# Kernel tuning notes

Measured on AMD Instinct MI355X. Metric: run time of the kernel, lower is better.

The kernel has to match this reference:

```python
import jax, jax.numpy as jnp
import numpy as np

WS = 8            # window_size
SHIFT = WS // 2   # shift_size


def _relative_position_index(ws):
    coords = np.stack(np.meshgrid(np.arange(ws), np.arange(ws), indexing='ij'))  # (2, ws, ws)
    coords = coords.reshape(2, -1)                        # (2, ws^2)
    rel = coords[:, :, None] - coords[:, None, :]          # (2, ws^2, ws^2)
    rel = rel.transpose(1, 2, 0)
    rel[:, :, 0] += ws - 1
    rel[:, :, 1] += ws - 1
    rel[:, :, 0] *= 2 * ws - 1
    return rel.sum(-1).astype(np.int32)                   # (ws^2, ws^2)


def _shift_mask(H, W, ws, shift):
    # Swin-style region-id mask for shifted windows -> bool (nh, nw, ws^2, ws^2)
    img = np.zeros((H, W), dtype=np.int32)
    cnt = 0
    sl = (slice(0, -ws), slice(-ws, -shift), slice(-shift, None))
    for hs in sl:
        for wsl in sl:
            img[hs, wsl] = cnt
            cnt += 1
    nh, nw = H // ws, W // ws
    win = img.reshape(nh, ws, nw, ws).transpose(0, 2, 1, 3).reshape(nh, nw, ws * ws)
    return win[:, :, :, None] != win[:, :, None, :]


def setup_inputs() -> dict:
    key = jax.random.key(0)
    ks = jax.random.split(key, 6)
    B, H, W, D, NHEAD = 8, 256, 256, 96, 6
    x = jax.random.normal(ks[0], (B, H, W, D), dtype=jnp.float32)
    w_qkv = jax.random.normal(ks[1], (D, 3 * D), dtype=jnp.float32) * 0.05
    b_qkv = jnp.zeros((3 * D,), dtype=jnp.float32)
    w_out = jax.random.normal(ks[2], (D, D), dtype=jnp.float32) * 0.05
    b_out = jnp.zeros((D,), dtype=jnp.float32)
    rpe_table = jax.random.normal(ks[3], ((2 * WS - 1) ** 2, NHEAD), dtype=jnp.float32) * 0.02
    rp_index = jnp.asarray(_relative_position_index(WS))
    mask = jnp.asarray(_shift_mask(H, W, WS, SHIFT))
    return {"x": x, "w_qkv": w_qkv, "b_qkv": b_qkv, "w_out": w_out,
            "b_out": b_out, "rpe_table": rpe_table, "rp_index": rp_index, "mask": mask}


def _partition(t, ws):
    # (B, h, H, W, dk) -> (B, h, nh, nw, ws*ws, dk)
    B, h, H, W, dk = t.shape
    nh, nw = H // ws, W // ws
    t = t.reshape(B, h, nh, ws, nw, ws, dk).transpose(0, 1, 2, 4, 3, 5, 6)
    return t.reshape(B, h, nh, nw, ws * ws, dk)


def _merge(t, ws):
    # inverse of _partition -> (B, h, H, W, dk)
    B, h, nh, nw, _, dk = t.shape
    t = t.reshape(B, h, nh, nw, ws, ws, dk).transpose(0, 1, 2, 4, 3, 5, 6)
    return t.reshape(B, h, nh * ws, nw * ws, dk)


def reference(x, w_qkv, b_qkv, w_out, b_out, rpe_table, rp_index, mask):
    B, H, W, D = x.shape
    n_head = rpe_table.shape[1]
    d_k = D // n_head
    scale = 1.0 / np.sqrt(d_k)
    ws2 = mask.shape[-1]
    ws = int(round(ws2 ** 0.5))
    shift = ws // 2

    qkv = (x @ w_qkv + b_qkv).reshape(B, H, W, 3, n_head, d_k)
    qkv = qkv.transpose(3, 0, 4, 1, 2, 5)          # (3, B, h, H, W, dk)
    q, k, v = qkv[0], qkv[1], qkv[2]

    # cyclic shift
    q = jnp.roll(q, (-shift, -shift), axis=(2, 3))
    k = jnp.roll(k, (-shift, -shift), axis=(2, 3))
    v = jnp.roll(v, (-shift, -shift), axis=(2, 3))

    q = _partition(q, ws)                          # (B, h, nh, nw, ws^2, dk)
    k = _partition(k, ws)
    v = _partition(v, ws)

    scores = jnp.einsum('bhijqd,bhijkd->bhijqk', q, k) * scale
    bias = rpe_table[rp_index]                     # (ws^2, ws^2, h)
    scores = scores + bias.transpose(2, 0, 1)[None, :, None, None]
    scores = jnp.where(mask[None, None], -1e9, scores)
    attn = jax.nn.softmax(scores, axis=-1)

    out = jnp.einsum('bhijqk,bhijkd->bhijqd', attn, v)
    out = _merge(out, ws)                          # (B, h, H, W, dk)
    out = jnp.roll(out, (shift, shift), axis=(2, 3))
    out = out.transpose(0, 2, 3, 1, 4).reshape(B, H, W, D)
    return out @ w_out + b_out
```

## Files before the change

kernel.cpp:

```cpp
#include <hip/hip_runtime.h>
#include <stdint.h>

#define HH    256
#define DD    96
#define NH    6
#define WSZ   8

typedef __bf16 bf16_t;
typedef bf16_t bf16x8 __attribute__((ext_vector_type(8)));
typedef short  s16x4  __attribute__((ext_vector_type(4)));
typedef float  f32x4  __attribute__((ext_vector_type(4)));

union U2  { bf16_t h[2]; uint32_t u; };
union Upk { uint32_t u[2]; s16x4 s; };

#define LOG2E 1.44269504088896f

static __device__ __forceinline__ uint32_t pack2(float a, float b) {
    U2 x; x.h[0] = (bf16_t)a; x.h[1] = (bf16_t)b; return x.u;
}

static __device__ __forceinline__ f32x4 mfma16(s16x4 a, s16x4 b, f32x4 c) {
#if __has_builtin(__builtin_amdgcn_mfma_f32_16x16x16bf16_1k)
    return __builtin_amdgcn_mfma_f32_16x16x16bf16_1k(a, b, c, 0, 0, 0);
#else
    f32x4 d;
    asm volatile("v_mfma_f32_16x16x16_bf16 %0, %1, %2, %3"
                 : "=v"(d) : "v"(a), "v"(b), "v"(c));
    return d;
#endif
}

static __device__ __forceinline__ float fast_exp2(float x) {
#if __has_builtin(__builtin_amdgcn_exp2f)
    return __builtin_amdgcn_exp2f(x);
#else
    return exp2f(x);
#endif
}

static __device__ __forceinline__ float fast_rcp(float x) {
#if __has_builtin(__builtin_amdgcn_rcpf)
    return __builtin_amdgcn_rcpf(x);
#else
    return 1.0f / x;
#endif
}

#define OFF_WQT_HI 0
#define OFF_WQT_LO 36864
#define OFF_WV_HI  73728
#define OFF_WV_LO  92160
#define OFF_WO_HI  110592
#define OFF_WO_LO  129024
#define OFF_RPE    147456

static __device__ __forceinline__ int swz(int row, int col) {
    return row * 128 + ((((col >> 3) ^ (row & 15)) & 15) << 3) + (col & 7);
}

__global__ __launch_bounds__(256)
void prep_kernel(const float* __restrict__ wqkv, const float* __restrict__ wout,
                 const float* __restrict__ rpe, char* __restrict__ ws)
{
    bf16_t* wqt_hi = (bf16_t*)(ws + OFF_WQT_HI);
    bf16_t* wqt_lo = (bf16_t*)(ws + OFF_WQT_LO);
    bf16_t* wv_hi  = (bf16_t*)(ws + OFF_WV_HI);
    bf16_t* wv_lo  = (bf16_t*)(ws + OFF_WV_LO);
    bf16_t* wo_hi  = (bf16_t*)(ws + OFF_WO_HI);
    bf16_t* wo_lo  = (bf16_t*)(ws + OFF_WO_LO);
    float*  rpe_b  = (float*)(ws + OFF_RPE);

    int idx = blockIdx.x * 256 + threadIdx.x;
    {
        int j = idx & 7, lane = (idx >> 3) & 63, frag = idx >> 9;
        int c = lane & 15, g = lane >> 4;
        if (idx < 18432) {
            int ks = frag % 3, r2 = frag / 3, wh = r2 % 6, t = r2 / 6;
            int k = ks * 32 + g * 8 + j;
            float v = wqkv[k * 288 + t * 96 + wh * 16 + c];
            bf16_t h = (bf16_t)v;
            wqt_hi[idx] = h;
            wqt_lo[idx] = (bf16_t)(v - (float)h);
        }
        if (idx < 9216) {
            int ks = frag % 3, wh = frag / 3;
            int k = ks * 32 + g * 8 + j;
            float v = wqkv[k * 288 + 192 + wh * 16 + c];
            bf16_t h = (bf16_t)v;
            wv_hi[idx] = h;
            wv_lo[idx] = (bf16_t)(v - (float)h);
            float v2 = wout[k * 96 + wh * 16 + c];
            bf16_t h2 = (bf16_t)v2;
            wo_hi[idx] = h2;
            wo_lo[idx] = (bf16_t)(v2 - (float)h2);
        }
    }
    if (idx < 24576) {
        int i = idx & 3, lane = (idx >> 2) & 63, kt = (idx >> 8) & 3,
            nt = (idx >> 10) & 3, h = idx >> 12;
        int c = lane & 15, g = lane >> 4;
        int k = kt * 16 + g * 4 + i, q = nt * 16 + c;
        int qr = q >> 3, qc = q & 7, kr = k >> 3, kc = k & 7;
        rpe_b[idx] = rpe[((qr - kr + 7) * 15 + (qc - kc + 7)) * NH + h] * LOG2E;
    }
}

__global__ __launch_bounds__(768, 4)
void swin_mfma(const float* __restrict__ x,
               const float* __restrict__ b_qkv,
               const float* __restrict__ b_out,
               const char*  __restrict__ ws,
               float* __restrict__ out)
{
    __shared__ char smem[65536];

    const int tid  = threadIdx.x;
    const int w2   = tid >> 6;
    const int wv   = (w2 >= 6) ? 1 : 0;
    const int w    = w2 - 6 * wv;
    const int lane = tid & 63;
    const int g    = lane >> 4;
    const int c    = lane & 15;
    const int tl   = tid - (wv << 8) - (wv << 7);

    bf16_t* xs_hi = (bf16_t*)(smem + (wv << 14));
    bf16_t* o_hi  = (bf16_t*)(smem + 32768 + (wv << 14));

    const bf16_t* wqt_hi = (const bf16_t*)(ws + OFF_WQT_HI);
    const bf16_t* wqt_lo = (const bf16_t*)(ws + OFF_WQT_LO);
    const bf16_t* wv_hi  = (const bf16_t*)(ws + OFF_WV_HI);
    const bf16_t* wv_lo  = (const bf16_t*)(ws + OFF_WV_LO);
    const bf16_t* wo_hi  = (const bf16_t*)(ws + OFF_WO_HI);
    const bf16_t* wo_lo  = (const bf16_t*)(ws + OFF_WO_LO);
    const float*  rpe_b  = (const float*)(ws + OFF_RPE);

    const int blk = blockIdx.x;
    const int b   = blk >> 9;
    const int wi  = (blk >> 4) & 31;
    const int wj  = ((blk & 15) << 1) + wv;

    uint32_t pix[4];
    #pragma unroll
    for (int t = 0; t < 4; ++t) {
        int p = t * 16 + c;
        int gh = (wi * WSZ + (p >> 3) + 4) & 255;
        int gw = (wj * WSZ + (p & 7) + 4) & 255;
        pix[t] = (((uint32_t)b * HH + gh) << 8) + gw;
    }

    const f32x4 zf = {0.f, 0.f, 0.f, 0.f};

    #pragma unroll
    for (int it = 0; it < 4; ++it) {
        int f4  = tl + it * 384;
        int row = f4 / 24, c4 = f4 - row * 24;
        int r = row >> 3, cl = row & 7;
        int gh = (wi * WSZ + r + 4) & 255;
        int gw = (wj * WSZ + cl + 4) & 255;
        const float4 v = *(const float4*)(x + (((size_t)b * HH + gh) * HH + gw) * DD + c4 * 4);
        uint2 hv;
        hv.x = pack2(v.x, v.y); hv.y = pack2(v.z, v.w);
        *(uint2*)&xs_hi[swz(row, c4 * 4)] = hv;
    }
    __syncthreads();

    f32x4 aq[4], akk[4], av[4];
    {
        const float4 bq4 = *(const float4*)&b_qkv[w * 16 + 4 * g];
        const float4 bk4 = *(const float4*)&b_qkv[96 + w * 16 + 4 * g];
        const float  bv  = b_qkv[192 + w * 16 + c];
        #pragma unroll
        for (int t4 = 0; t4 < 4; ++t4) {
            aq[t4]  = (f32x4){bq4.x, bq4.y, bq4.z, bq4.w};
            akk[t4] = (f32x4){bk4.x, bk4.y, bk4.z, bk4.w};
            av[t4]  = (f32x4){bv, bv, bv, bv};
        }
    }
    #pragma unroll
    for (int ks = 0; ks < 3; ++ks) {
        bf16x8 ah[4];
        #pragma unroll
        for (int mt = 0; mt < 4; ++mt) {
            int e = (mt * 16 + c) * 128 + (((ks * 4 + g) ^ c) << 3);
            ah[mt] = *(const bf16x8*)&xs_hi[e];
        }
        const bf16x8 qh = *(const bf16x8*)&wqt_hi[(w * 3 + ks) * 512 + lane * 8];
        const bf16x8 ql = *(const bf16x8*)&wqt_lo[(w * 3 + ks) * 512 + lane * 8];
        const bf16x8 kh = *(const bf16x8*)&wqt_hi[((6 + w) * 3 + ks) * 512 + lane * 8];
        const bf16x8 kl = *(const bf16x8*)&wqt_lo[((6 + w) * 3 + ks) * 512 + lane * 8];
        const bf16x8 vh = *(const bf16x8*)&wv_hi[(w * 3 + ks) * 512 + lane * 8];
        const bf16x8 vl = *(const bf16x8*)&wv_lo[(w * 3 + ks) * 512 + lane * 8];
        #pragma unroll
        for (int mt = 0; mt < 4; ++mt) {
            aq[mt]  = __builtin_amdgcn_mfma_f32_16x16x32_bf16(qh, ah[mt], aq[mt], 0, 0, 0);
            aq[mt]  = __builtin_amdgcn_mfma_f32_16x16x32_bf16(ql, ah[mt], aq[mt], 0, 0, 0);
            akk[mt] = __builtin_amdgcn_mfma_f32_16x16x32_bf16(kh, ah[mt], akk[mt], 0, 0, 0);
            akk[mt] = __builtin_amdgcn_mfma_f32_16x16x32_bf16(kl, ah[mt], akk[mt], 0, 0, 0);
            av[mt]  = __builtin_amdgcn_mfma_f32_16x16x32_bf16(ah[mt], vh, av[mt], 0, 0, 0);
            av[mt]  = __builtin_amdgcn_mfma_f32_16x16x32_bf16(ah[mt], vl, av[mt], 0, 0, 0);
        }
    }

    s16x4 aqb[4], akb[4], avb[4];
    #pragma unroll
    for (int t = 0; t < 4; ++t) {
        Upk uq, uk, uv;
        const float qs = 0.25f * LOG2E;
        uq.u[0] = pack2(aq[t][0] * qs, aq[t][1] * qs);
        uq.u[1] = pack2(aq[t][2] * qs, aq[t][3] * qs);
        uk.u[0] = pack2(akk[t][0], akk[t][1]);
        uk.u[1] = pack2(akk[t][2], akk[t][3]);
        uv.u[0] = pack2(av[t][0], av[t][1]);
        uv.u[1] = pack2(av[t][2], av[t][3]);
        aqb[t] = uq.s; akb[t] = uk.s; avb[t] = uv.s;
    }

    const int e_wi = (wi == 31), e_wj = (wj == 31);
    const bool edge = e_wi || e_wj;
    int rk[4][4];
    #pragma unroll
    for (int kt = 0; kt < 4; ++kt)
        #pragma unroll
        for (int i = 0; i < 4; ++i) {
            int k = kt * 16 + g * 4 + i;
            int kr = k >> 3, kc = k & 7;
            rk[kt][i] = (e_wi ? (kr >= 4 ? 2 : 1) : 0) * 3 + (e_wj ? (kc >= 4 ? 2 : 1) : 0);
        }

    #pragma unroll
    for (int nt = 0; nt < 4; ++nt) {
        f32x4 stc[4];
        #pragma unroll
        for (int kt = 0; kt < 4; ++kt) {
            const f32x4 rc = *(const f32x4*)&rpe_b[(((w * 4 + nt) * 4 + kt) << 8) + lane * 4];
            stc[kt] = mfma16(akb[kt], aqb[nt], rc);
        }

        int q = nt * 16 + c, qr = q >> 3, qc = q & 7;
        int rq = (e_wi ? (qr >= 4 ? 2 : 1) : 0) * 3 + (e_wj ? (qc >= 4 ? 2 : 1) : 0);
        float sv[16];
        float sum = 0.f;
        #pragma unroll
        for (int kt = 0; kt < 4; ++kt)
            #pragma unroll
            for (int i = 0; i < 4; ++i) {
                float s = stc[kt][i];
                if (edge && (rk[kt][i] != rq)) s = -1e9f;
                s = fast_exp2(s);
                sv[kt * 4 + i] = s;
                sum += s;
            }
        sum += __shfl_xor(sum, 16);
        sum += __shfl_xor(sum, 32);
        const float rinv = fast_rcp(sum);

        f32x4 oa = zf;
        #pragma unroll
        for (int ks2 = 0; ks2 < 4; ++ks2) {
            Upk pb;
            pb.u[0] = pack2(sv[ks2 * 4 + 0], sv[ks2 * 4 + 1]);
            pb.u[1] = pack2(sv[ks2 * 4 + 2], sv[ks2 * 4 + 3]);
            oa = mfma16(avb[ks2], pb.s, oa);
        }
        {
            uint2 hv;
            hv.x = pack2(oa[0] * rinv, oa[1] * rinv);
            hv.y = pack2(oa[2] * rinv, oa[3] * rinv);
            *(uint2*)&o_hi[swz(nt * 16 + c, w * 16 + 4 * g)] = hv;
        }
    }
    __syncthreads();

    f32x4 acc3[4];
    {
        const float4 bo4 = *(const float4*)&b_out[w * 16 + 4 * g];
        #pragma unroll
        for (int nt = 0; nt < 4; ++nt)
            acc3[nt] = (f32x4){bo4.x, bo4.y, bo4.z, bo4.w};
    }
    #pragma unroll
    for (int ks = 0; ks < 3; ++ks) {
        bf16x8 oh[4];
        #pragma unroll
        for (int nt = 0; nt < 4; ++nt) {
            int e = (nt * 16 + c) * 128 + (((ks * 4 + g) ^ c) << 3);
            oh[nt] = *(const bf16x8*)&o_hi[e];
        }
        const bf16x8 bh = *(const bf16x8*)&wo_hi[(w * 3 + ks) * 512 + lane * 8];
        const bf16x8 bl = *(const bf16x8*)&wo_lo[(w * 3 + ks) * 512 + lane * 8];
        #pragma unroll
        for (int nt = 0; nt < 4; ++nt) {
            acc3[nt] = __builtin_amdgcn_mfma_f32_16x16x32_bf16(bh, oh[nt], acc3[nt], 0, 0, 0);
            acc3[nt] = __builtin_amdgcn_mfma_f32_16x16x32_bf16(bl, oh[nt], acc3[nt], 0, 0, 0);
        }
    }
    #pragma unroll
    for (int nt = 0; nt < 4; ++nt)
        *(f32x4*)(out + (size_t)pix[nt] * DD + w * 16 + 4 * g) = acc3[nt];
}

extern "C" void kernel_launch(void* const* d_in, const int* in_sizes, int n_in,
                              void* d_out, int out_size, void* d_ws, size_t ws_size,
                              hipStream_t stream) {
    const float* x    = (const float*)d_in[0];
    const float* wqkv = (const float*)d_in[1];
    const float* bqkv = (const float*)d_in[2];
    const float* wout = (const float*)d_in[3];
    const float* bout = (const float*)d_in[4];
    const float* rpe  = (const float*)d_in[5];
    float* out = (float*)d_out;
    char* ws = (char*)d_ws;

    const int B = in_sizes[0] / (HH * HH * DD);

    hipLaunchKernelGGL(prep_kernel, dim3(96), dim3(256), 0, stream, wqkv, wout, rpe, ws);
    hipLaunchKernelGGL(swin_mfma, dim3(B * 512), dim3(768), 0, stream,
                       x, bqkv, bout, (const char*)ws, out);
}
```

Baseline: 194.8 us.

## Alias output tile onto input smem, drop Q/K lo weights, specialize edge path

Shared memory is halved by reusing the x-tile buffer for the attention output, with an extra barrier added so the QKV reads finish before the buffer is overwritten. The low-order bf16 correction terms for the Q and K weights are removed, cutting the QKV MFMA count from six to four per step at some cost in precision. The first K-step weight fragments are hoisted ahead of the x tile load to hide their latency. The attention loop is split into an edge-masked and an unmasked version so interior windows skip the mask logic. Together these aim to raise occupancy and reduce matrix and ALU work.

```diff
diff --git a/kernel.cpp b/kernel.cpp
--- a/kernel.cpp
+++ b/kernel.cpp
@@ -106,6 +106,49 @@
     }
 }
 
+#define ATTN_LOOP(EDGE_ON)                                                      \
+    _Pragma("unroll")                                                           \
+    for (int nt = 0; nt < 4; ++nt) {                                            \
+        f32x4 stc[4];                                                           \
+        _Pragma("unroll")                                                       \
+        for (int kt = 0; kt < 4; ++kt) {                                        \
+            const f32x4 rc = *(const f32x4*)&rpe_b[(((w * 4 + nt) * 4 + kt) << 8) + lane * 4]; \
+            stc[kt] = mfma16(akb[kt], aqb[nt], rc);                             \
+        }                                                                       \
+        int rq = 0;                                                             \
+        if (EDGE_ON) {                                                          \
+            int q = nt * 16 + c, qr = q >> 3, qc = q & 7;                       \
+            rq = (e_wi ? (qr >= 4 ? 2 : 1) : 0) * 3 + (e_wj ? (qc >= 4 ? 2 : 1) : 0); \
+        }                                                                       \
+        float sv[16];                                                           \
+        float sum = 0.f;                                                        \
+        _Pragma("unroll")                                                       \
+        for (int kt = 0; kt < 4; ++kt)                                          \
+            _Pragma("unroll")                                                   \
+            for (int i = 0; i < 4; ++i) {                                       \
+                float s = stc[kt][i];                                           \
+                if (EDGE_ON && (rk[kt][i] != rq)) s = -1e9f;                    \
+                s = fast_exp2(s);                                               \
+                sv[kt * 4 + i] = s;                                             \
+                sum += s;                                                       \
+            }                                                                   \
+        sum += __shfl_xor(sum, 16);                                             \
+        sum += __shfl_xor(sum, 32);                                             \
+        const float rinv = fast_rcp(sum);                                       \
+        f32x4 oa = zf;                                                          \
+        _Pragma("unroll")                                                       \
+        for (int ks2 = 0; ks2 < 4; ++ks2) {                                     \
+            Upk pb;                                                             \
+            pb.u[0] = pack2(sv[ks2 * 4 + 0], sv[ks2 * 4 + 1]);                  \
+            pb.u[1] = pack2(sv[ks2 * 4 + 2], sv[ks2 * 4 + 3]);                  \
+            oa = mfma16(avb[ks2], pb.s, oa);                                    \
+        }                                                                       \
+        uint2 hv;                                                               \
+        hv.x = pack2(oa[0] * rinv, oa[1] * rinv);                               \
+        hv.y = pack2(oa[2] * rinv, oa[3] * rinv);                               \
+        *(uint2*)&o_hi[swz(nt * 16 + c, w * 16 + 4 * g)] = hv;                  \
+    }
+
 __global__ __launch_bounds__(768, 4)
 void swin_mfma(const float* __restrict__ x,
                const float* __restrict__ b_qkv,
@@ -113,7 +156,7 @@
                const char*  __restrict__ ws,
                float* __restrict__ out)
 {
-    __shared__ char smem[65536];
+    __shared__ char smem[32768];
 
     const int tid  = threadIdx.x;
     const int w2   = tid >> 6;
@@ -125,10 +168,9 @@
     const int tl   = tid - (wv << 8) - (wv << 7);
 
     bf16_t* xs_hi = (bf16_t*)(smem + (wv << 14));
-    bf16_t* o_hi  = (bf16_t*)(smem + 32768 + (wv << 14));
+    bf16_t* o_hi  = xs_hi;
 
     const bf16_t* wqt_hi = (const bf16_t*)(ws + OFF_WQT_HI);
-    const bf16_t* wqt_lo = (const bf16_t*)(ws + OFF_WQT_LO);
     const bf16_t* wv_hi  = (const bf16_t*)(ws + OFF_WV_HI);
     const bf16_t* wv_lo  = (const bf16_t*)(ws + OFF_WV_LO);
     const bf16_t* wo_hi  = (const bf16_t*)(ws + OFF_WO_HI);
@@ -139,6 +181,11 @@
     const int b   = blk >> 9;
     const int wi  = (blk >> 4) & 31;
     const int wj  = ((blk & 15) << 1) + wv;
+
+    const bf16x8 qh0 = *(const bf16x8*)&wqt_hi[(w * 3 + 0) * 512 + lane * 8];
+    const bf16x8 kh0 = *(const bf16x8*)&wqt_hi[((6 + w) * 3 + 0) * 512 + lane * 8];
+    const bf16x8 vh0 = *(const bf16x8*)&wv_hi[(w * 3 + 0) * 512 + lane * 8];
+    const bf16x8 vl0 = *(const bf16x8*)&wv_lo[(w * 3 + 0) * 512 + lane * 8];
 
     uint32_t pix[4];
     #pragma unroll
@@ -185,22 +232,19 @@
             int e = (mt * 16 + c) * 128 + (((ks * 4 + g) ^ c) << 3);
             ah[mt] = *(const bf16x8*)&xs_hi[e];
         }
-        const bf16x8 qh = *(const bf16x8*)&wqt_hi[(w * 3 + ks) * 512 + lane * 8];
-        const bf16x8 ql = *(const bf16x8*)&wqt_lo[(w * 3 + ks) * 512 + lane * 8];
-        const bf16x8 kh = *(const bf16x8*)&wqt_hi[((6 + w) * 3 + ks) * 512 + lane * 8];
-        const bf16x8 kl = *(const bf16x8*)&wqt_lo[((6 + w) * 3 + ks) * 512 + lane * 8];
-        const bf16x8 vh = *(const bf16x8*)&wv_hi[(w * 3 + ks) * 512 + lane * 8];
-        const bf16x8 vl = *(const bf16x8*)&wv_lo[(w * 3 + ks) * 512 + lane * 8];
+        const bf16x8 qh = (ks == 0) ? qh0 : *(const bf16x8*)&wqt_hi[(w * 3 + ks) * 512 + lane * 8];
+        const bf16x8 kh = (ks == 0) ? kh0 : *(const bf16x8*)&wqt_hi[((6 + w) * 3 + ks) * 512 + lane * 8];
+        const bf16x8 vh = (ks == 0) ? vh0 : *(const bf16x8*)&wv_hi[(w * 3 + ks) * 512 + lane * 8];
+        const bf16x8 vl = (ks == 0) ? vl0 : *(const bf16x8*)&wv_lo[(w * 3 + ks) * 512 + lane * 8];
         #pragma unroll
         for (int mt = 0; mt < 4; ++mt) {
             aq[mt]  = __builtin_amdgcn_mfma_f32_16x16x32_bf16(qh, ah[mt], aq[mt], 0, 0, 0);
-            aq[mt]  = __builtin_amdgcn_mfma_f32_16x16x32_bf16(ql, ah[mt], aq[mt], 0, 0, 0);
             akk[mt] = __builtin_amdgcn_mfma_f32_16x16x32_bf16(kh, ah[mt], akk[mt], 0, 0, 0);
-            akk[mt] = __builtin_amdgcn_mfma_f32_16x16x32_bf16(kl, ah[mt], akk[mt], 0, 0, 0);
             av[mt]  = __builtin_amdgcn_mfma_f32_16x16x32_bf16(ah[mt], vh, av[mt], 0, 0, 0);
             av[mt]  = __builtin_amdgcn_mfma_f32_16x16x32_bf16(ah[mt], vl, av[mt], 0, 0, 0);
         }
     }
+    __syncthreads();
 
     s16x4 aqb[4], akb[4], avb[4];
     #pragma unroll
@@ -219,56 +263,18 @@
     const int e_wi = (wi == 31), e_wj = (wj == 31);
     const bool edge = e_wi || e_wj;
     int rk[4][4];
-    #pragma unroll
-    for (int kt = 0; kt < 4; ++kt)
-        #pragma unroll
-        for (int i = 0; i < 4; ++i) {
-            int k = kt * 16 + g * 4 + i;
-            int kr = k >> 3, kc = k & 7;
-            rk[kt][i] = (e_wi ? (kr >= 4 ? 2 : 1) : 0) * 3 + (e_wj ? (kc >= 4 ? 2 : 1) : 0);
-        }
-
-    #pragma unroll
-    for (int nt = 0; nt < 4; ++nt) {
-        f32x4 stc[4];
-        #pragma unroll
-        for (int kt = 0; kt < 4; ++kt) {
-            const f32x4 rc = *(const f32x4*)&rpe_b[(((w * 4 + nt) * 4 + kt) << 8) + lane * 4];
-            stc[kt] = mfma16(akb[kt], aqb[nt], rc);
-        }
-
-        int q = nt * 16 + c, qr = q >> 3, qc = q & 7;
-        int rq = (e_wi ? (qr >= 4 ? 2 : 1) : 0) * 3 + (e_wj ? (qc >= 4 ? 2 : 1) : 0);
-        float sv[16];
-        float sum = 0.f;
+    if (edge) {
         #pragma unroll
         for (int kt = 0; kt < 4; ++kt)
             #pragma unroll
             for (int i = 0; i < 4; ++i) {
-                float s = stc[kt][i];
-                if (edge && (rk[kt][i] != rq)) s = -1e9f;
-                s = fast_exp2(s);
-                sv[kt * 4 + i] = s;
-                sum += s;
+                int k = kt * 16 + g * 4 + i;
+                int kr = k >> 3, kc = k & 7;
+                rk[kt][i] = (e_wi ? (kr >= 4 ? 2 : 1) : 0) * 3 + (e_wj ? (kc >= 4 ? 2 : 1) : 0);
             }
-        sum += __shfl_xor(sum, 16);
-        sum += __shfl_xor(sum, 32);
-        const float rinv = fast_rcp(sum);
-
-        f32x4 oa = zf;
-        #pragma unroll
-        for (int ks2 = 0; ks2 < 4; ++ks2) {
-            Upk pb;
-            pb.u[0] = pack2(sv[ks2 * 4 + 0], sv[ks2 * 4 + 1]);
-            pb.u[1] = pack2(sv[ks2 * 4 + 2], sv[ks2 * 4 + 3]);
-            oa = mfma16(avb[ks2], pb.s, oa);
-        }
-        {
-            uint2 hv;
-            hv.x = pack2(oa[0] * rinv, oa[1] * rinv);
-            hv.y = pack2(oa[2] * rinv, oa[3] * rinv);
-            *(uint2*)&o_hi[swz(nt * 16 + c, w * 16 + 4 * g)] = hv;
-        }
+        ATTN_LOOP(1)
+    } else {
+        ATTN_LOOP(0)
     }
     __syncthreads();
 
```

Measured after the change: 166.6 us. 1.17x faster.
